# Optimization experiments

Hardware: AMD Instinct MI355X
Metric: run time of the kernel (lower is better)

Reference implementation:

```python
import jax, jax.numpy as jnp
import numpy as np

K_NN = 3  # pointnet2 relation default k=3


def setup_inputs() -> dict:
    key = jax.random.key(0)
    k1, k2, k3 = jax.random.split(key, 3)
    B, N, S, C = 4, 16384, 4096, 256
    q = jax.random.normal(k1, (B, N, 3), dtype=jnp.float32)
    k = jax.random.normal(k2, (B, S, 3), dtype=jnp.float32)
    v = jax.random.normal(k3, (B, S, C), dtype=jnp.float32)
    return {"q": q, "k": k, "v": v}


def reference(q, k, v):
    # squared pairwise distance: ||q||^2 - 2 q.k + ||k||^2  -> [B, N, S]
    d = (
        jnp.sum(q * q, axis=-1, keepdims=True)
        - 2.0 * jnp.einsum("bnd,bsd->bns", q, k)
        + jnp.sum(k * k, axis=-1)[:, None, :]
    )
    # 3 nearest neighbors (smallest distances)
    neg_d, idx = jax.lax.top_k(-d, K_NN)          # [B, N, 3]
    dists = -neg_d
    recip = 1.0 / (dists + 1e-8)
    weight = recip / jnp.sum(recip, axis=-1, keepdims=True)  # [B, N, 3]
    # score is zero except at idx; scatter+dense matmul == gather-weighted sum
    B = q.shape[0]
    vg = v[jnp.arange(B)[:, None, None], idx]     # [B, N, 3, C]
    extract = jnp.einsum("bnk,bnkc->bnc", weight, vg)  # [B, N, C]
    return jnp.transpose(extract, (0, 2, 1))      # [B, C, N] (embed is identity)
```

## Files before the change

kernel.cpp:

```cpp
#include <hip/hip_runtime.h>

#define BB 4
#define NN 16384
#define SS 4096
#define CC 256
#define RQ 2
#define TLD 132

typedef float f32x4 __attribute__((ext_vector_type(4)));

__device__ __forceinline__ bool lexlt(float da, int ia, float db, int ib) {
  return (da < db) || ((da == db) && (ia < ib));
}

__global__ __launch_bounds__(256, 4) void fused_kernel(
    const float* __restrict__ qg, const float* __restrict__ kg,
    const float* __restrict__ vg, float* __restrict__ outg) {
#pragma clang fp contract(off)
  __shared__ __align__(16) char buf[64 * TLD * 4];
  __shared__ float sw[64][3];
  __shared__ int si[64][3];
  float4* kpts = (float4*)buf;
  float* tile = (float*)buf;
  float* md = (float*)buf;
  int* mi = (int*)(buf + 3072);

  const int tid = threadIdx.x;
  const int bid = blockIdx.x;
  const int b = (bid >> 1) & 3;
  const int nh = bid & 1;
  const int nblk = bid >> 3;
  const int n0 = (nh * 128 + nblk) << 6;
  const int qlane = tid & 31;
  const int g = tid >> 5;

  float qx[RQ], qy[RQ], qz[RQ], qq[RQ];
  float d0[RQ], d1[RQ], d2[RQ];
  int i0[RQ], i1[RQ], i2[RQ];
#pragma unroll
  for (int j = 0; j < RQ; ++j) {
    int n = n0 + qlane + 32 * j;
    const float* qp = qg + ((long)b * NN + n) * 3;
    qx[j] = qp[0]; qy[j] = qp[1]; qz[j] = qp[2];
    qq[j] = (qx[j] * qx[j] + qy[j] * qy[j]) + qz[j] * qz[j];
    d0[j] = 3.4e38f; d1[j] = 3.4e38f; d2[j] = 3.4e38f;
    i0[j] = 0; i1[j] = 0; i2[j] = 0;
  }

  for (int r = 0; r < 4; ++r) {
    {
      const float* kb = kg + ((long)b * SS + (long)r * 1024) * 3;
      const float4* src = (const float4*)kb + tid * 3;
      float4 f0 = src[0], f1 = src[1], f2 = src[2];
      float px[4] = {f0.x, f0.w, f1.z, f2.y};
      float py[4] = {f0.y, f1.x, f1.w, f2.z};
      float pz[4] = {f0.z, f1.y, f2.x, f2.w};
#pragma unroll
      for (int m = 0; m < 4; ++m) {
        float kk = (px[m] * px[m] + py[m] * py[m]) + pz[m] * pz[m];
        kpts[tid * 4 + m] = make_float4(px[m], py[m], pz[m], kk);
      }
    }
    __syncthreads();

    const int sbase = r * 1024 + g * 128;
#pragma unroll 2
    for (int i = 0; i < 128; ++i) {
      float4 kp = kpts[g * 128 + i];
      const int s = sbase + i;
#pragma unroll
      for (int j = 0; j < RQ; ++j) {
        float dot = (qx[j] * kp.x + qy[j] * kp.y) + qz[j] * kp.z;
        float d = __builtin_fmaf(dot, -2.0f, qq[j]) + kp.w;
        bool k2 = d < d2[j];
        bool k1 = d < d1[j];
        bool k0 = d < d0[j];
        float nd2 = __builtin_amdgcn_fmed3f(d, d1[j], d2[j]);
        float nd1 = __builtin_amdgcn_fmed3f(d, d0[j], d1[j]);
        float nd0 = fminf(d, d0[j]);
        i2[j] = k1 ? i1[j] : (k2 ? s : i2[j]);
        i1[j] = k0 ? i0[j] : (k1 ? s : i1[j]);
        i0[j] = k0 ? s : i0[j];
        d2[j] = nd2; d1[j] = nd1; d0[j] = nd0;
      }
    }
    __syncthreads();
  }

#pragma unroll
  for (int j = 0; j < RQ; ++j) {
    float E0 = __shfl_xor(d0[j], 32), E1 = __shfl_xor(d1[j], 32), E2 = __shfl_xor(d2[j], 32);
    int F0 = __shfl_xor(i0[j], 32), F1 = __shfl_xor(i1[j], 32), F2 = __shfl_xor(i2[j], 32);
    float A0 = d0[j], A1 = d1[j], A2 = d2[j];
    int B0 = i0[j], B1 = i1[j], B2 = i2[j];
    bool t = lexlt(E0, F0, A0, B0);
    float r0 = t ? E0 : A0; int s0 = t ? F0 : B0;
    float nA0 = t ? A0 : A1, nA1 = t ? A1 : A2;
    int nB0 = t ? B0 : B1, nB1 = t ? B1 : B2;
    float nE0 = t ? E1 : E0, nE1 = t ? E2 : E1;
    int nF0 = t ? F1 : F0, nF1 = t ? F2 : F1;
    bool u = lexlt(nE0, nF0, nA0, nB0);
    float r1 = u ? nE0 : nA0; int s1 = u ? nF0 : nB0;
    float mA0 = u ? nA0 : nA1; int mB0 = u ? nB0 : nB1;
    float mE0 = u ? nE1 : nE0; int mF0 = u ? nF1 : nF0;
    bool w = lexlt(mE0, mF0, mA0, mB0);
    float r2 = w ? mE0 : mA0; int s2 = w ? mF0 : mB0;
    d0[j] = r0; d1[j] = r1; d2[j] = r2;
    i0[j] = s0; i1[j] = s1; i2[j] = s2;
  }

  if ((tid & 63) < 32) {
    const int wv = tid >> 6;
#pragma unroll
    for (int j = 0; j < RQ; ++j) {
      int base = (((wv * 32) + qlane) * RQ + j) * 3;
      md[base + 0] = d0[j]; md[base + 1] = d1[j]; md[base + 2] = d2[j];
      mi[base + 0] = i0[j]; mi[base + 1] = i1[j]; mi[base + 2] = i2[j];
    }
  }
  __syncthreads();

  if (tid < 64) {
    const int ql = tid & 31, jj = tid >> 5;
    float D0 = 3.4e38f, D1 = 3.4e38f, D2 = 3.4e38f;
    int I0 = -1, I1 = -1, I2 = -1;
    for (int wv = 0; wv < 4; ++wv) {
      int base = ((wv * 32 + ql) * RQ + jj) * 3;
      for (int r = 0; r < 3; ++r) {
        float d = md[base + r];
        int s = mi[base + r];
        if (lexlt(d, s, D2, I2)) {
          if (lexlt(d, s, D1, I1)) {
            D2 = D1; I2 = I1;
            if (lexlt(d, s, D0, I0)) { D1 = D0; I1 = I0; D0 = d; I0 = s; }
            else { D1 = d; I1 = s; }
          } else { D2 = d; I2 = s; }
        }
      }
    }
    float r0 = 1.0f / (D0 + 1e-8f);
    float r1 = 1.0f / (D1 + 1e-8f);
    float r2 = 1.0f / (D2 + 1e-8f);
    float rs = (r0 + r1) + r2;
    sw[tid][0] = r0 / rs; sw[tid][1] = r1 / rs; sw[tid][2] = r2 / rs;
    si[tid][0] = I0; si[tid][1] = I1; si[tid][2] = I2;
  }
  __syncthreads();

  const int wv4 = tid >> 6;
  const int lane = tid & 63;
  const int qh = lane >> 5;
  const int slot = lane & 31;
  const int nf = tid & 15;
  const int cb0 = tid >> 4;

#pragma unroll
  for (int chunk = 0; chunk < 2; ++chunk) {
    const float* vb = vg + (long)b * SS * CC + (chunk << 7);
#pragma unroll 4
    for (int it = 0; it < 8; ++it) {
      int qs = wv4 * 16 + it * 2 + qh;
      float w0 = sw[qs][0], w1 = sw[qs][1], w2 = sw[qs][2];
      const float4* r0p = (const float4*)(vb + (long)si[qs][0] * CC);
      const float4* r1p = (const float4*)(vb + (long)si[qs][1] * CC);
      const float4* r2p = (const float4*)(vb + (long)si[qs][2] * CC);
      float4 a0 = r0p[slot], a1 = r1p[slot], a2 = r2p[slot];
      float4 acc;
      acc.x = (w0 * a0.x + w1 * a1.x) + w2 * a2.x;
      acc.y = (w0 * a0.y + w1 * a1.y) + w2 * a2.y;
      acc.z = (w0 * a0.z + w1 * a1.z) + w2 * a2.z;
      acc.w = (w0 * a0.w + w1 * a1.w) + w2 * a2.w;
      int col = (slot ^ ((qs >> 2) & 7)) << 2;
      *(float4*)&tile[qs * TLD + col] = acc;
    }
    __syncthreads();
    {
      const int q0 = nf << 2;
#pragma unroll 2
      for (int it = 0; it < 8; ++it) {
        int cl = cb0 + it * 16;
        int cch = (chunk << 7) + cl;
        int colw = (((cl >> 2) ^ (nf & 7)) << 2) | (cl & 3);
        f32x4 val;
        val.x = tile[(q0 + 0) * TLD + colw];
        val.y = tile[(q0 + 1) * TLD + colw];
        val.z = tile[(q0 + 2) * TLD + colw];
        val.w = tile[(q0 + 3) * TLD + colw];
        __builtin_nontemporal_store(
            val, (f32x4*)&outg[((long)(b * CC + cch)) * NN + n0 + q0]);
      }
    }
    __syncthreads();
  }
}

extern "C" void kernel_launch(void* const* d_in, const int* in_sizes, int n_in,
                              void* d_out, int out_size, void* d_ws, size_t ws_size,
                              hipStream_t stream) {
  const float* q = (const float*)d_in[0];
  const float* k = (const float*)d_in[1];
  const float* v = (const float*)d_in[2];
  float* out = (float*)d_out;
  hipLaunchKernelGGL(fused_kernel, dim3(1024), dim3(256), 0, stream, q, k, v, out);
}
```

Baseline: 241.5 us.

## Split key prep into separate kernel and skip top-k updates via wave-any test

Adds a prep kernel that packs key points with their squared norms into workspace, then restructures the fused kernel to 128 threads with one query per lane and each wave scanning half the keys. The top-3 insertion is guarded by a wave-wide any() test, so the whole wave skips the update when no lane improves. The gather/transpose stage is rewritten with a padded tile instead of XOR swizzling. This trades per-point ALU work for a branch per candidate and an extra kernel launch, and it halves the threads per block.

```diff
diff --git a/kernel.cpp b/kernel.cpp
--- a/kernel.cpp
+++ b/kernel.cpp
@@ -4,8 +4,7 @@
 #define NN 16384
 #define SS 4096
 #define CC 256
-#define RQ 2
-#define TLD 132
+#define TLD 261
 
 typedef float f32x4 __attribute__((ext_vector_type(4)));
 
@@ -13,122 +12,89 @@
   return (da < db) || ((da == db) && (ia < ib));
 }
 
-__global__ __launch_bounds__(256, 4) void fused_kernel(
-    const float* __restrict__ qg, const float* __restrict__ kg,
+__global__ __launch_bounds__(256) void prep_kernel(const float* __restrict__ kg,
+                                                   float4* __restrict__ cand) {
+#pragma clang fp contract(off)
+  int gid = blockIdx.x * 256 + threadIdx.x;
+  int b = gid >> 12, s = gid & 4095;
+  const float* kp = kg + ((long)b * SS + s) * 3;
+  float x = kp[0], y = kp[1], z = kp[2];
+  float kk = (x * x + y * y) + z * z;
+  cand[(long)b * SS + s] = make_float4(x, y, z, kk);
+}
+
+__global__ __launch_bounds__(128, 2) void fused_kernel(
+    const float* __restrict__ qg, const float4* __restrict__ cand,
     const float* __restrict__ vg, float* __restrict__ outg) {
 #pragma clang fp contract(off)
-  __shared__ __align__(16) char buf[64 * TLD * 4];
+  __shared__ __align__(16) char buf[32 * TLD * 4];
   __shared__ float sw[64][3];
   __shared__ int si[64][3];
-  float4* kpts = (float4*)buf;
+  float4* kst = (float4*)buf;
   float* tile = (float*)buf;
-  float* md = (float*)buf;
-  int* mi = (int*)(buf + 3072);
+  float* wm = (float*)buf;
+  int* im = (int*)(buf + 1536);
 
   const int tid = threadIdx.x;
   const int bid = blockIdx.x;
   const int b = (bid >> 1) & 3;
-  const int nh = bid & 1;
-  const int nblk = bid >> 3;
-  const int n0 = (nh * 128 + nblk) << 6;
-  const int qlane = tid & 31;
-  const int g = tid >> 5;
+  const int n0 = (((bid & 1) << 7) + (bid >> 3)) << 6;
+  const int w = tid >> 6;
+  const int lane = tid & 63;
 
-  float qx[RQ], qy[RQ], qz[RQ], qq[RQ];
-  float d0[RQ], d1[RQ], d2[RQ];
-  int i0[RQ], i1[RQ], i2[RQ];
+  const float* qp = qg + ((long)b * NN + n0 + lane) * 3;
+  float qx = qp[0], qy = qp[1], qz = qp[2];
+  float qq = (qx * qx + qy * qy) + qz * qz;
+  float d0 = 3.4e38f, d1 = 3.4e38f, d2 = 3.4e38f;
+  int i0 = 0, i1 = 0, i2 = 0;
+
+  const float4* csrc = cand + (long)b * SS + w * 2048;
+  for (int c = 0; c < 4; ++c) {
+    float4 tmp[8];
 #pragma unroll
-  for (int j = 0; j < RQ; ++j) {
-    int n = n0 + qlane + 32 * j;
-    const float* qp = qg + ((long)b * NN + n) * 3;
-    qx[j] = qp[0]; qy[j] = qp[1]; qz[j] = qp[2];
-    qq[j] = (qx[j] * qx[j] + qy[j] * qy[j]) + qz[j] * qz[j];
-    d0[j] = 3.4e38f; d1[j] = 3.4e38f; d2[j] = 3.4e38f;
-    i0[j] = 0; i1[j] = 0; i2[j] = 0;
+    for (int m = 0; m < 8; ++m) tmp[m] = csrc[c * 512 + lane + 64 * m];
+    __syncthreads();
+#pragma unroll
+    for (int m = 0; m < 8; ++m) kst[w * 512 + lane + 64 * m] = tmp[m];
+    __syncthreads();
+    const int sbase = w * 2048 + c * 512;
+#pragma unroll 4
+    for (int i = 0; i < 512; ++i) {
+      float4 kp = kst[w * 512 + i];
+      float dot = (qx * kp.x + qy * kp.y) + qz * kp.z;
+      float d = __builtin_fmaf(dot, -2.0f, qq) + kp.w;
+      if (__builtin_expect(__any(d < d2), 0)) {
+        const int s = sbase + i;
+        bool k2 = d < d2;
+        bool k1 = d < d1;
+        bool k0 = d < d0;
+        float nd2 = __builtin_amdgcn_fmed3f(d, d1, d2);
+        float nd1 = __builtin_amdgcn_fmed3f(d, d0, d1);
+        float nd0 = fminf(d, d0);
+        i2 = k1 ? i1 : (k2 ? s : i2);
+        i1 = k0 ? i0 : (k1 ? s : i1);
+        i0 = k0 ? s : i0;
+        d2 = nd2; d1 = nd1; d0 = nd0;
+      }
+    }
   }
 
-  for (int r = 0; r < 4; ++r) {
-    {
-      const float* kb = kg + ((long)b * SS + (long)r * 1024) * 3;
-      const float4* src = (const float4*)kb + tid * 3;
-      float4 f0 = src[0], f1 = src[1], f2 = src[2];
-      float px[4] = {f0.x, f0.w, f1.z, f2.y};
-      float py[4] = {f0.y, f1.x, f1.w, f2.z};
-      float pz[4] = {f0.z, f1.y, f2.x, f2.w};
-#pragma unroll
-      for (int m = 0; m < 4; ++m) {
-        float kk = (px[m] * px[m] + py[m] * py[m]) + pz[m] * pz[m];
-        kpts[tid * 4 + m] = make_float4(px[m], py[m], pz[m], kk);
-      }
-    }
-    __syncthreads();
-
-    const int sbase = r * 1024 + g * 128;
-#pragma unroll 2
-    for (int i = 0; i < 128; ++i) {
-      float4 kp = kpts[g * 128 + i];
-      const int s = sbase + i;
-#pragma unroll
-      for (int j = 0; j < RQ; ++j) {
-        float dot = (qx[j] * kp.x + qy[j] * kp.y) + qz[j] * kp.z;
-        float d = __builtin_fmaf(dot, -2.0f, qq[j]) + kp.w;
-        bool k2 = d < d2[j];
-        bool k1 = d < d1[j];
-        bool k0 = d < d0[j];
-        float nd2 = __builtin_amdgcn_fmed3f(d, d1[j], d2[j]);
-        float nd1 = __builtin_amdgcn_fmed3f(d, d0[j], d1[j]);
-        float nd0 = fminf(d, d0[j]);
-        i2[j] = k1 ? i1[j] : (k2 ? s : i2[j]);
-        i1[j] = k0 ? i0[j] : (k1 ? s : i1[j]);
-        i0[j] = k0 ? s : i0[j];
-        d2[j] = nd2; d1[j] = nd1; d0[j] = nd0;
-      }
-    }
-    __syncthreads();
-  }
-
-#pragma unroll
-  for (int j = 0; j < RQ; ++j) {
-    float E0 = __shfl_xor(d0[j], 32), E1 = __shfl_xor(d1[j], 32), E2 = __shfl_xor(d2[j], 32);
-    int F0 = __shfl_xor(i0[j], 32), F1 = __shfl_xor(i1[j], 32), F2 = __shfl_xor(i2[j], 32);
-    float A0 = d0[j], A1 = d1[j], A2 = d2[j];
-    int B0 = i0[j], B1 = i1[j], B2 = i2[j];
-    bool t = lexlt(E0, F0, A0, B0);
-    float r0 = t ? E0 : A0; int s0 = t ? F0 : B0;
-    float nA0 = t ? A0 : A1, nA1 = t ? A1 : A2;
-    int nB0 = t ? B0 : B1, nB1 = t ? B1 : B2;
-    float nE0 = t ? E1 : E0, nE1 = t ? E2 : E1;
-    int nF0 = t ? F1 : F0, nF1 = t ? F2 : F1;
-    bool u = lexlt(nE0, nF0, nA0, nB0);
-    float r1 = u ? nE0 : nA0; int s1 = u ? nF0 : nB0;
-    float mA0 = u ? nA0 : nA1; int mB0 = u ? nB0 : nB1;
-    float mE0 = u ? nE1 : nE0; int mF0 = u ? nF1 : nF0;
-    bool w = lexlt(mE0, mF0, mA0, mB0);
-    float r2 = w ? mE0 : mA0; int s2 = w ? mF0 : mB0;
-    d0[j] = r0; d1[j] = r1; d2[j] = r2;
-    i0[j] = s0; i1[j] = s1; i2[j] = s2;
-  }
-
-  if ((tid & 63) < 32) {
-    const int wv = tid >> 6;
-#pragma unroll
-    for (int j = 0; j < RQ; ++j) {
-      int base = (((wv * 32) + qlane) * RQ + j) * 3;
-      md[base + 0] = d0[j]; md[base + 1] = d1[j]; md[base + 2] = d2[j];
-      mi[base + 0] = i0[j]; mi[base + 1] = i1[j]; mi[base + 2] = i2[j];
-    }
+  __syncthreads();
+  {
+    int base = (w * 64 + lane) * 3;
+    wm[base + 0] = d0; wm[base + 1] = d1; wm[base + 2] = d2;
+    im[base + 0] = i0; im[base + 1] = i1; im[base + 2] = i2;
   }
   __syncthreads();
 
   if (tid < 64) {
-    const int ql = tid & 31, jj = tid >> 5;
     float D0 = 3.4e38f, D1 = 3.4e38f, D2 = 3.4e38f;
     int I0 = -1, I1 = -1, I2 = -1;
-    for (int wv = 0; wv < 4; ++wv) {
-      int base = ((wv * 32 + ql) * RQ + jj) * 3;
+    for (int wv = 0; wv < 2; ++wv) {
+      int base = (wv * 64 + tid) * 3;
       for (int r = 0; r < 3; ++r) {
-        float d = md[base + r];
-        int s = mi[base + r];
+        float d = wm[base + r];
+        int s = im[base + r];
         if (lexlt(d, s, D2, I2)) {
           if (lexlt(d, s, D1, I1)) {
             D2 = D1; I2 = I1;
@@ -147,48 +113,37 @@
   }
   __syncthreads();
 
-  const int wv4 = tid >> 6;
-  const int lane = tid & 63;
-  const int qh = lane >> 5;
-  const int slot = lane & 31;
-  const int nf = tid & 15;
-  const int cb0 = tid >> 4;
-
+  const float* vb = vg + (long)b * SS * CC;
 #pragma unroll
   for (int chunk = 0; chunk < 2; ++chunk) {
-    const float* vb = vg + (long)b * SS * CC + (chunk << 7);
-#pragma unroll 4
-    for (int it = 0; it < 8; ++it) {
-      int qs = wv4 * 16 + it * 2 + qh;
+#pragma unroll 2
+    for (int it = 0; it < 16; ++it) {
+      int qs = chunk * 32 + w * 16 + it;
       float w0 = sw[qs][0], w1 = sw[qs][1], w2 = sw[qs][2];
       const float4* r0p = (const float4*)(vb + (long)si[qs][0] * CC);
       const float4* r1p = (const float4*)(vb + (long)si[qs][1] * CC);
       const float4* r2p = (const float4*)(vb + (long)si[qs][2] * CC);
-      float4 a0 = r0p[slot], a1 = r1p[slot], a2 = r2p[slot];
+      float4 a0 = r0p[lane], a1 = r1p[lane], a2 = r2p[lane];
       float4 acc;
       acc.x = (w0 * a0.x + w1 * a1.x) + w2 * a2.x;
       acc.y = (w0 * a0.y + w1 * a1.y) + w2 * a2.y;
       acc.z = (w0 * a0.z + w1 * a1.z) + w2 * a2.z;
       acc.w = (w0 * a0.w + w1 * a1.w) + w2 * a2.w;
-      int col = (slot ^ ((qs >> 2) & 7)) << 2;
-      *(float4*)&tile[qs * TLD + col] = acc;
+      *(float4*)&tile[(w * 16 + it) * TLD + lane * 4] = acc;
     }
     __syncthreads();
-    {
-      const int q0 = nf << 2;
 #pragma unroll 2
-      for (int it = 0; it < 8; ++it) {
-        int cl = cb0 + it * 16;
-        int cch = (chunk << 7) + cl;
-        int colw = (((cl >> 2) ^ (nf & 7)) << 2) | (cl & 3);
-        f32x4 val;
-        val.x = tile[(q0 + 0) * TLD + colw];
-        val.y = tile[(q0 + 1) * TLD + colw];
-        val.z = tile[(q0 + 2) * TLD + colw];
-        val.w = tile[(q0 + 3) * TLD + colw];
-        __builtin_nontemporal_store(
-            val, (f32x4*)&outg[((long)(b * CC + cch)) * NN + n0 + q0]);
-      }
+    for (int it = 0; it < 16; ++it) {
+      int item = it * 128 + tid;
+      int nf = item & 7;
+      int cch = item >> 3;
+      f32x4 val;
+      val.x = tile[(nf * 4 + 0) * TLD + cch];
+      val.y = tile[(nf * 4 + 1) * TLD + cch];
+      val.z = tile[(nf * 4 + 2) * TLD + cch];
+      val.w = tile[(nf * 4 + 3) * TLD + cch];
+      __builtin_nontemporal_store(
+          val, (f32x4*)&outg[((long)(b * CC + cch)) * NN + n0 + chunk * 32 + nf * 4]);
     }
     __syncthreads();
   }
@@ -201,5 +156,7 @@
   const float* k = (const float*)d_in[1];
   const float* v = (const float*)d_in[2];
   float* out = (float*)d_out;
-  hipLaunchKernelGGL(fused_kernel, dim3(1024), dim3(256), 0, stream, q, k, v, out);
+  float4* cand = (float4*)d_ws;
+  hipLaunchKernelGGL(prep_kernel, dim3(64), dim3(256), 0, stream, k, cand);
+  hipLaunchKernelGGL(fused_kernel, dim3(1024), dim3(128), 0, stream, q, cand, v, out);
 }
```

New measurement: 251.1 us. 4.0% more time.
